# Kernel optimization log

Measured on AMD Instinct MI355X. Metric: run time of the kernel, lower is better.

## Reference

```python
import jax, jax.numpy as jnp
import numpy as np

N = 50000      # nodes
E = 1600000    # edges
M = 2          # modalities
DIN, H1, LAT, DEC, HID, NC = 2000, 500, 128, 64, 64, 16
EPS = 1e-5


def setup_inputs() -> dict:
    key = jax.random.key(0)
    ks = jax.random.split(key, 24)
    s = 0.02
    return {
        "x": jax.random.normal(ks[0], (M, N, DIN), jnp.float32),
        "src": jax.random.randint(ks[1], (E,), 0, N, jnp.int32),
        "dst": jax.random.randint(ks[2], (E,), 0, N, jnp.int32),
        "W1": jax.random.normal(ks[3], (M, DIN, H1), jnp.float32) * s,
        "b1": jax.random.normal(ks[4], (M, H1), jnp.float32) * s,
        "g1": jax.random.uniform(ks[5], (M, H1), jnp.float32) + 0.5,
        "be1": jax.random.normal(ks[6], (M, H1), jnp.float32) * s,
        "m1": jax.random.normal(ks[7], (M, H1), jnp.float32) * s,
        "v1": jax.random.uniform(ks[8], (M, H1), jnp.float32) + 0.5,
        "W2": jax.random.normal(ks[9], (M, H1, LAT), jnp.float32) * s,
        "b2": jax.random.normal(ks[10], (M, LAT), jnp.float32) * s,
        "g2": jax.random.uniform(ks[11], (M, LAT), jnp.float32) + 0.5,
        "be2": jax.random.normal(ks[12], (M, LAT), jnp.float32) * s,
        "m2": jax.random.normal(ks[13], (M, LAT), jnp.float32) * s,
        "v2": jax.random.uniform(ks[14], (M, LAT), jnp.float32) + 0.5,
        "Wd": jax.random.normal(ks[15], (M, LAT, DEC), jnp.float32) * s,
        "bd": jax.random.normal(ks[16], (M, DEC), jnp.float32) * s,
        "Wg1": jax.random.normal(ks[17], (DEC, HID), jnp.float32) * s,
        "bg1": jax.random.normal(ks[18], (HID,), jnp.float32) * s,
        "Wg2": jax.random.normal(ks[19], (HID, NC), jnp.float32) * s,
        "bg2": jax.random.normal(ks[20], (NC,), jnp.float32) * s,
    }


def _bn(h, g, b, m, v):
    # inference-mode BatchNorm1d; params broadcast over [M, 1, F]
    return (h - m[:, None, :]) * jax.lax.rsqrt(v[:, None, :] + EPS) * g[:, None, :] + b[:, None, :]


def reference(x, src, dst, W1, b1, g1, be1, m1, v1, W2, b2, g2, be2, m2, v2,
              Wd, bd, Wg1, bg1, Wg2, bg2):
    # --- multi-modal encoders (dropout = identity at eval) ---
    h = jnp.einsum('mnd,mdh->mnh', x, W1) + b1[:, None, :]        # [M,N,500]
    h = _bn(h, g1, be1, m1, v1)
    h = jnp.einsum('mnh,mhl->mnl', h, W2) + b2[:, None, :]        # [M,N,LAT]
    h = _bn(h, g2, be2, m2, v2)
    dec = jnp.einsum('mnl,mld->mnd', h, Wd) + bd[:, None, :]      # [M,N,DEC]
    node_features = jnp.mean(dec, axis=0)                         # [N,DEC]

    # --- GraphConv (DGL norm='both'): D_out^{-1/2} on src, D_in^{-1/2} on dst ---
    ones = jnp.ones(src.shape[0], jnp.float32)
    deg_out = jax.ops.segment_sum(ones, src, num_segments=N)
    deg_in = jax.ops.segment_sum(ones, dst, num_segments=N)
    c_src = jax.lax.rsqrt(jnp.clip(deg_out, 1.0))[:, None]
    c_dst = jax.lax.rsqrt(jnp.clip(deg_in, 1.0))[:, None]

    def gconv(feat, W, b):
        msg = (feat * c_src)[src]                                 # [E,F]
        agg = jax.ops.segment_sum(msg, dst, num_segments=N)       # [N,F]
        return (agg * c_dst) @ W + b

    h = jax.nn.relu(gconv(node_features, Wg1, bg1))               # [N,HID]
    score = gconv(h, Wg2, bg2)                                    # [N,NC]
    return score
```

## Files before the change

### kernel.cpp

```cpp
#include <hip/hip_runtime.h>

#define NN 50000
#define EE 1600000
#define MM 2
#define DIN 2000
#define H1 500
#define LAT 128
#define DECF 64
#define KTOT (MM*DIN)
#define KSTEPS (KTOT/32)
#define NTILES (NN/16)
#define GEMM_BLKS 768
#define DEG_BLKS 256
#define EPSBN 1e-5f

typedef float f32x4 __attribute__((ext_vector_type(4)));
typedef short short8v __attribute__((ext_vector_type(8)));
typedef unsigned int u32x2 __attribute__((ext_vector_type(2)));

__device__ __forceinline__ unsigned int pkbf(float a, float b){
  unsigned int ua = __float_as_uint(a), ub = __float_as_uint(b);
  ua = (ua + 0x7FFFu + ((ua>>16)&1u)) >> 16;
  ub = (ub + 0x7FFFu + ((ub>>16)&1u)) & 0xFFFF0000u;
  return ua | ub;
}
__device__ __forceinline__ unsigned short pk1(float a){
  unsigned int u = __float_as_uint(a);
  return (unsigned short)((u + 0x7FFFu + ((u>>16)&1u)) >> 16);
}
__device__ __forceinline__ float bfe0(unsigned int w){ return __uint_as_float(w<<16); }
__device__ __forceinline__ float bfe1(unsigned int w){ return __uint_as_float(w & 0xFFFF0000u); }

__global__ __launch_bounds__(256) void prepA(const float* __restrict__ W2,const float* __restrict__ Wd,
                      const float* __restrict__ g2,const float* __restrict__ v2,
                      float* __restrict__ T){
  __shared__ float a2[LAT];
  int m = (blockIdx.x*4) / H1;
  if (threadIdx.x < LAT)
    a2[threadIdx.x] = g2[m*LAT+threadIdx.x]*rsqrtf(v2[m*LAT+threadIdx.x]+EPSBN);
  __syncthreads();
  int g = blockIdx.x*256 + threadIdx.x;
  int d = g & 63; int mk = g >> 6; int k = mk % H1;
  const float* w2 = W2 + (size_t)(m*H1 + k)*LAT;
  const float* wd = Wd + (size_t)m*LAT*DECF + d;
  float acc = 0.f;
  for (int l = 0; l < LAT; ++l) acc += w2[l]*a2[l]*wd[(size_t)l*DECF];
  T[g] = acc;
}

__global__ __launch_bounds__(256) void prepB(const float* __restrict__ W1,const float* __restrict__ g1,
                      const float* __restrict__ v1,const float* __restrict__ T,
                      unsigned short* __restrict__ WB){
  __shared__ float a1[H1];
  int m = (blockIdx.x*4) / DIN;
  for (int k = threadIdx.x; k < H1; k += 256)
    a1[k] = g1[m*H1+k]*rsqrtf(v1[m*H1+k]+EPSBN);
  __syncthreads();
  int g = blockIdx.x*256 + threadIdx.x;
  int d = g & 63; int mi = g >> 6; int i = mi % DIN;
  const float* w1 = W1 + (size_t)(m*DIN + i)*H1;
  const float* t  = T + (size_t)m*H1*DECF + d;
  float acc = 0.f;
  for (int k = 0; k < H1; ++k) acc += w1[k]*a1[k]*t[(size_t)k*DECF];
  acc *= 0.5f;
  unsigned int u = __float_as_uint(acc);
  unsigned short bf = (unsigned short)((u + 0x7FFFu + ((u>>16)&1u)) >> 16);
  int kc = m*DIN + i;
  int s = kc >> 5, kl = kc & 31;
  int laneB = ((kl>>3)<<4) | (d & 15);
  int t4 = d >> 4;
  WB[((size_t)((s*4 + t4)*64 + laneB))*8 + (kl & 7)] = bf;
}

__global__ void prepC(const float* __restrict__ b1,const float* __restrict__ g1,const float* __restrict__ be1,
                      const float* __restrict__ m1,const float* __restrict__ v1,
                      const float* __restrict__ b2,const float* __restrict__ g2,const float* __restrict__ be2,
                      const float* __restrict__ m2,const float* __restrict__ v2,
                      const float* __restrict__ T,const float* __restrict__ Wd,
                      const float* __restrict__ bd, float* __restrict__ cbar){
  __shared__ float part[128];
  int d = threadIdx.x & 63, h = threadIdx.x >> 6;
  float s = 0.f;
  for (int m = 0; m < MM; ++m){
    if (h == 0) s += bd[m*DECF + d];
    const float* t = T + (size_t)m*H1*DECF + d;
    for (int k = h*(H1/2); k < (h+1)*(H1/2); ++k){
      float a = g1[m*H1+k]*rsqrtf(v1[m*H1+k]+EPSBN);
      float c = (b1[m*H1+k]-m1[m*H1+k])*a + be1[m*H1+k];
      s += c*t[(size_t)k*DECF];
    }
    const float* wd = Wd + (size_t)m*LAT*DECF + d;
    for (int l = h*(LAT/2); l < (h+1)*(LAT/2); ++l){
      float a = g2[m*LAT+l]*rsqrtf(v2[m*LAT+l]+EPSBN);
      float c = (b2[m*LAT+l]-m2[m*LAT+l])*a + be2[m*LAT+l];
      s += c*wd[(size_t)l*DECF];
    }
  }
  part[threadIdx.x] = s;
  __syncthreads();
  if (h == 0) cbar[d] = 0.5f*(part[d] + part[64+d]);
}

__global__ __launch_bounds__(1024) void scan1(const int* __restrict__ deg, int* __restrict__ rp,
                      int* __restrict__ bsum, int n){
  __shared__ int sm[1024];
  int i = blockIdx.x*1024 + threadIdx.x;
  int v = (i < n) ? deg[i] : 0;
  sm[threadIdx.x] = v; __syncthreads();
  for (int off=1; off<1024; off<<=1){
    int t = (threadIdx.x >= off) ? sm[threadIdx.x-off] : 0;
    __syncthreads();
    sm[threadIdx.x] += t;
    __syncthreads();
  }
  if (i < n) rp[i] = sm[threadIdx.x] - v;
  if (threadIdx.x == 1023) bsum[blockIdx.x] = sm[1023];
}

__global__ void scan3n(int* __restrict__ rp, const int* __restrict__ bsum,
                       const int* __restrict__ dout, const int* __restrict__ din,
                       float* __restrict__ csrc, float* __restrict__ cdst){
  int i = blockIdx.x*blockDim.x + threadIdx.x;
  if (i >= NN) return;
  int b = i >> 10;
  int base = 0;
  for (int j = 0; j < b; ++j) base += bsum[j];
  rp[i] += base;
  if (i == NN-1) rp[NN] = EE;
  int a = dout[i]; if (a < 1) a = 1;
  int dd = din[i]; if (dd < 1) dd = 1;
  csrc[i] = rsqrtf((float)a);
  cdst[i] = rsqrtf((float)dd);
}

__global__ void scatk(const int* __restrict__ src,const int* __restrict__ dst,
                      const int* __restrict__ rp,int* __restrict__ cur,int* __restrict__ ss){
  int e = blockIdx.x*blockDim.x + threadIdx.x;
  if (e >= EE) return;
  int d = dst[e];
  int p = rp[d] + atomicAdd(&cur[d], 1);
  ss[p] = src[e];
}

__global__ __launch_bounds__(256,4) void gemm_deg(
    const float* __restrict__ x, const short8v* __restrict__ WB,
    const float* __restrict__ cbar,
    unsigned short* __restrict__ nfb, int* __restrict__ ticket,
    const int* __restrict__ src, const int* __restrict__ dst,
    int* __restrict__ dout, int* __restrict__ din)
{
  if (blockIdx.x >= GEMM_BLKS){
    int t0 = (blockIdx.x - GEMM_BLKS)*256 + threadIdx.x;
    for (int e = t0; e < EE; e += 256*DEG_BLKS){
      atomicAdd(&dout[src[e]], 1);
      atomicAdd(&din[dst[e]], 1);
    }
    return;
  }
  const int lane = threadIdx.x & 63;
  const int r = lane & 15;
  const int kg = (lane >> 4) << 3;
  const int rg = (lane >> 4) << 2;
  const float cb0 = cbar[r], cb1 = cbar[16+r], cb2 = cbar[32+r], cb3 = cbar[48+r];

  while (true){
    int t = 0;
    if (lane == 0) t = atomicAdd(ticket, 1);
    t = __shfl(t, 0, 64);
    if (t >= NTILES) break;
    const int n0 = t*16;
    const float* xrow = x + (size_t)(n0 + r) * DIN;

    f32x4 acc0 = {0.f,0.f,0.f,0.f}, acc1 = acc0, acc2 = acc0, acc3 = acc0;
    f32x4 A0c, A1c; short8v B0c, B1c, B2c, B3c;
    {
      const float* p = xrow + kg;
      A0c = *(const f32x4*)p; A1c = *(const f32x4*)(p+4);
      const short8v* bp = WB + lane;
      B0c = bp[0]; B1c = bp[64]; B2c = bp[128]; B3c = bp[192];
    }
    for (int s = 0; s < KSTEPS-1; ++s){
      f32x4 A0n, A1n; short8v B0n, B1n, B2n, B3n;
      {
        int kr = (s+1)*32 + kg;
        const float* p = (kr < DIN) ? (xrow + kr)
                                    : (xrow + (size_t)(NN-1)*DIN + kr);
        A0n = *(const f32x4*)p; A1n = *(const f32x4*)(p+4);
        const short8v* bp = WB + (size_t)(s+1)*256 + lane;
        B0n = bp[0]; B1n = bp[64]; B2n = bp[128]; B3n = bp[192];
      }
      union { short8v v; unsigned int u[4]; } AF;
      AF.u[0]=pkbf(A0c[0],A0c[1]); AF.u[1]=pkbf(A0c[2],A0c[3]);
      AF.u[2]=pkbf(A1c[0],A1c[1]); AF.u[3]=pkbf(A1c[2],A1c[3]);
      acc0 = __builtin_amdgcn_mfma_f32_16x16x32_bf16(AF.v, B0c, acc0, 0,0,0);
      acc1 = __builtin_amdgcn_mfma_f32_16x16x32_bf16(AF.v, B1c, acc1, 0,0,0);
      acc2 = __builtin_amdgcn_mfma_f32_16x16x32_bf16(AF.v, B2c, acc2, 0,0,0);
      acc3 = __builtin_amdgcn_mfma_f32_16x16x32_bf16(AF.v, B3c, acc3, 0,0,0);
      A0c=A0n; A1c=A1n; B0c=B0n; B1c=B1n; B2c=B2n; B3c=B3n;
    }
    {
      union { short8v v; unsigned int u[4]; } AF;
      AF.u[0]=pkbf(A0c[0],A0c[1]); AF.u[1]=pkbf(A0c[2],A0c[3]);
      AF.u[2]=pkbf(A1c[0],A1c[1]); AF.u[3]=pkbf(A1c[2],A1c[3]);
      acc0 = __builtin_amdgcn_mfma_f32_16x16x32_bf16(AF.v, B0c, acc0, 0,0,0);
      acc1 = __builtin_amdgcn_mfma_f32_16x16x32_bf16(AF.v, B1c, acc1, 0,0,0);
      acc2 = __builtin_amdgcn_mfma_f32_16x16x32_bf16(AF.v, B2c, acc2, 0,0,0);
      acc3 = __builtin_amdgcn_mfma_f32_16x16x32_bf16(AF.v, B3c, acc3, 0,0,0);
    }
    #pragma unroll
    for (int rr = 0; rr < 4; ++rr){
      int rowD = n0 + rg + rr;
      unsigned short* o = nfb + (size_t)rowD*64 + r;
      o[0]  = pk1(acc0[rr] + cb0);
      o[16] = pk1(acc1[rr] + cb1);
      o[32] = pk1(acc2[rr] + cb2);
      o[48] = pk1(acc3[rr] + cb3);
    }
  }
}

__global__ __launch_bounds__(512,4) void fgd1(const unsigned short* __restrict__ nfb,
                      const int* __restrict__ rp,const int* __restrict__ ss,
                      const float* __restrict__ Wg1,const float* __restrict__ bg1,
                      const float* __restrict__ csrc,const float* __restrict__ cdst,
                      unsigned short* __restrict__ hpb){
  __shared__ float W[64*64];
  for (int i = threadIdx.x; i < 64*64; i += 512) W[i] = Wg1[i];
  __syncthreads();
  int wave = threadIdx.x >> 6, lane = threadIdx.x & 63;
  int q = lane >> 4, cc = (lane & 15)*4;
  const int NW = 512*8;
  for (int n = blockIdx.x*8 + wave; n < NN; n += NW){
    int beg = rp[n], end = rp[n+1];
    f32x4 s4 = {0.f,0.f,0.f,0.f};
    int e = beg + q;
    for (; e + 12 < end; e += 16){
      int i0 = ss[e], i1 = ss[e+4], i2 = ss[e+8], i3 = ss[e+12];
      float c0 = csrc[i0], c1 = csrc[i1], c2 = csrc[i2], c3 = csrc[i3];
      u32x2 w0 = *(const u32x2*)(nfb + (size_t)i0*64 + cc);
      u32x2 w1 = *(const u32x2*)(nfb + (size_t)i1*64 + cc);
      u32x2 w2 = *(const u32x2*)(nfb + (size_t)i2*64 + cc);
      u32x2 w3 = *(const u32x2*)(nfb + (size_t)i3*64 + cc);
      s4.x += c0*bfe0(w0.x) + c1*bfe0(w1.x) + c2*bfe0(w2.x) + c3*bfe0(w3.x);
      s4.y += c0*bfe1(w0.x) + c1*bfe1(w1.x) + c2*bfe1(w2.x) + c3*bfe1(w3.x);
      s4.z += c0*bfe0(w0.y) + c1*bfe0(w1.y) + c2*bfe0(w2.y) + c3*bfe0(w3.y);
      s4.w += c0*bfe1(w0.y) + c1*bfe1(w1.y) + c2*bfe1(w2.y) + c3*bfe1(w3.y);
    }
    for (; e < end; e += 4){
      int i0 = ss[e]; float c0 = csrc[i0];
      u32x2 w0 = *(const u32x2*)(nfb + (size_t)i0*64 + cc);
      s4.x += c0*bfe0(w0.x); s4.y += c0*bfe1(w0.x);
      s4.z += c0*bfe0(w0.y); s4.w += c0*bfe1(w0.y);
    }
    s4.x += __shfl_xor(s4.x,16); s4.y += __shfl_xor(s4.y,16);
    s4.z += __shfl_xor(s4.z,16); s4.w += __shfl_xor(s4.w,16);
    s4.x += __shfl_xor(s4.x,32); s4.y += __shfl_xor(s4.y,32);
    s4.z += __shfl_xor(s4.z,32); s4.w += __shfl_xor(s4.w,32);
    float acc = 0.f;
    #pragma unroll
    for (int l16 = 0; l16 < 16; ++l16){
      acc += __shfl(s4.x,l16) * W[(4*l16+0)*64 + lane];
      acc += __shfl(s4.y,l16) * W[(4*l16+1)*64 + lane];
      acc += __shfl(s4.z,l16) * W[(4*l16+2)*64 + lane];
      acc += __shfl(s4.w,l16) * W[(4*l16+3)*64 + lane];
    }
    float h = fmaxf(cdst[n]*acc + bg1[lane], 0.f) * csrc[n];
    hpb[(size_t)n*64 + lane] = pk1(h);
  }
}

__global__ __launch_bounds__(512,4) void fgd2(const unsigned short* __restrict__ hpb,
                      const int* __restrict__ rp,const int* __restrict__ ss,
                      const float* __restrict__ Wg2,const float* __restrict__ bg2,
                      const float* __restrict__ cdst,float* __restrict__ score){
  __shared__ float W[64*16];
  for (int i = threadIdx.x; i < 64*16; i += 512) W[i] = Wg2[i];
  __syncthreads();
  int wave = threadIdx.x >> 6, lane = threadIdx.x & 63;
  int q = lane >> 4, cc = (lane & 15)*4;
  const int NW = 512*8;
  for (int n = blockIdx.x*8 + wave; n < NN; n += NW){
    int beg = rp[n], end = rp[n+1];
    f32x4 s4 = {0.f,0.f,0.f,0.f};
    int e = beg + q;
    for (; e + 12 < end; e += 16){
      int i0 = ss[e], i1 = ss[e+4], i2 = ss[e+8], i3 = ss[e+12];
      u32x2 w0 = *(const u32x2*)(hpb + (size_t)i0*64 + cc);
      u32x2 w1 = *(const u32x2*)(hpb + (size_t)i1*64 + cc);
      u32x2 w2 = *(const u32x2*)(hpb + (size_t)i2*64 + cc);
      u32x2 w3 = *(const u32x2*)(hpb + (size_t)i3*64 + cc);
      s4.x += bfe0(w0.x) + bfe0(w1.x) + bfe0(w2.x) + bfe0(w3.x);
      s4.y += bfe1(w0.x) + bfe1(w1.x) + bfe1(w2.x) + bfe1(w3.x);
      s4.z += bfe0(w0.y) + bfe0(w1.y) + bfe0(w2.y) + bfe0(w3.y);
      s4.w += bfe1(w0.y) + bfe1(w1.y) + bfe1(w2.y) + bfe1(w3.y);
    }
    for (; e < end; e += 4){
      u32x2 w0 = *(const u32x2*)(hpb + (size_t)ss[e]*64 + cc);
      s4.x += bfe0(w0.x); s4.y += bfe1(w0.x);
      s4.z += bfe0(w0.y); s4.w += bfe1(w0.y);
    }
    s4.x += __shfl_xor(s4.x,16); s4.y += __shfl_xor(s4.y,16);
    s4.z += __shfl_xor(s4.z,16); s4.w += __shfl_xor(s4.w,16);
    s4.x += __shfl_xor(s4.x,32); s4.y += __shfl_xor(s4.y,32);
    s4.z += __shfl_xor(s4.z,32); s4.w += __shfl_xor(s4.w,32);
    int c = lane & 15;
    float acc = 0.f;
    #pragma unroll
    for (int l16 = 0; l16 < 16; ++l16){
      acc += __shfl(s4.x,l16) * W[(4*l16+0)*16 + c];
      acc += __shfl(s4.y,l16) * W[(4*l16+1)*16 + c];
      acc += __shfl(s4.z,l16) * W[(4*l16+2)*16 + c];
      acc += __shfl(s4.w,l16) * W[(4*l16+3)*16 + c];
    }
    if (lane < 16) score[(size_t)n*16 + lane] = cdst[n]*acc + bg2[lane];
  }
}

extern "C" void kernel_launch(void* const* d_in, const int* in_sizes, int n_in,
                              void* d_out, int out_size, void* d_ws, size_t ws_size,
                              hipStream_t stream){
  const float* x   = (const float*)d_in[0];
  const int* src   = (const int*)d_in[1];
  const int* dst   = (const int*)d_in[2];
  const float* W1  = (const float*)d_in[3];
  const float* b1  = (const float*)d_in[4];
  const float* g1  = (const float*)d_in[5];
  const float* be1 = (const float*)d_in[6];
  const float* m1  = (const float*)d_in[7];
  const float* v1  = (const float*)d_in[8];
  const float* W2  = (const float*)d_in[9];
  const float* b2  = (const float*)d_in[10];
  const float* g2  = (const float*)d_in[11];
  const float* be2 = (const float*)d_in[12];
  const float* m2  = (const float*)d_in[13];
  const float* v2  = (const float*)d_in[14];
  const float* Wd  = (const float*)d_in[15];
  const float* bd  = (const float*)d_in[16];
  const float* Wg1 = (const float*)d_in[17];
  const float* bg1 = (const float*)d_in[18];
  const float* Wg2 = (const float*)d_in[19];
  const float* bg2 = (const float*)d_in[20];
  float* score = (float*)d_out;

  char* w = (char*)d_ws;
  size_t off = 0;
  auto alc = [&](size_t b){ size_t c = off; off += (b + 255) & ~(size_t)255; return c; };
  size_t o_dout = alc((size_t)NN*4), o_din = alc((size_t)NN*4), o_cur = alc((size_t)NN*4);
  size_t o_tick = alc(256);
  size_t zspan = off;
  size_t o_rp  = alc((size_t)(NN+1)*4), o_bsum = alc(256*4);
  size_t o_csrc = alc((size_t)NN*4), o_cdst = alc((size_t)NN*4);
  size_t o_T = alc((size_t)MM*H1*DECF*4), o_cbar = alc(DECF*4);
  size_t o_WB = alc((size_t)MM*DIN*DECF*2);
  size_t o_ss = alc((size_t)EE*4);
  size_t o_nf = alc((size_t)NN*64*2);
  size_t o_hp = alc((size_t)NN*64*2);

  int* dout = (int*)(w+o_dout); int* din = (int*)(w+o_din); int* cur = (int*)(w+o_cur);
  int* tick = (int*)(w+o_tick);
  int* rp = (int*)(w+o_rp); int* bsum = (int*)(w+o_bsum);
  float* csrc = (float*)(w+o_csrc); float* cdst = (float*)(w+o_cdst);
  float* T = (float*)(w+o_T); float* cbar = (float*)(w+o_cbar);
  unsigned short* WBu = (unsigned short*)(w+o_WB);
  int* ss = (int*)(w+o_ss);
  unsigned short* nfb = (unsigned short*)(w+o_nf);
  unsigned short* hpb = (unsigned short*)(w+o_hp);

  hipMemsetAsync(w, 0, zspan, stream);

  prepA<<<(MM*H1*DECF)/256,256,0,stream>>>(W2,Wd,g2,v2,T);
  prepB<<<(MM*DIN*DECF)/256,256,0,stream>>>(W1,g1,v1,T,WBu);
  prepC<<<1,128,0,stream>>>(b1,g1,be1,m1,v1,b2,g2,be2,m2,v2,T,Wd,bd,cbar);

  gemm_deg<<<GEMM_BLKS+DEG_BLKS,256,0,stream>>>(x,(const short8v*)(w+o_WB),cbar,
                                                nfb,tick,src,dst,dout,din);

  int nb = (NN+1023)/1024;
  scan1<<<nb,1024,0,stream>>>(din,rp,bsum,NN);
  scan3n<<<(NN+255)/256,256,0,stream>>>(rp,bsum,dout,din,csrc,cdst);
  scatk<<<(EE+255)/256,256,0,stream>>>(src,dst,rp,cur,ss);

  fgd1<<<512,512,0,stream>>>(nfb,rp,ss,Wg1,bg1,csrc,cdst,hpb);
  fgd2<<<512,512,0,stream>>>(hpb,rp,ss,Wg2,bg2,cdst,score);
}
```

Before: 702.7 us.

## Statically assign GEMM tiles and fold degree counting into every block; dual-node gather

The fused GEMM kernel drops the atomic ticket work queue and separate degree-counting blocks. Each of 782 blocks now counts degrees for its own contiguous edge slice and then computes one 16-row tile per wave, statically assigned. The two graph-conv gather kernels now process two nodes per wave at once, interleaving their neighbor loads to expose more memory-level parallelism. The trade-offs are possible load imbalance without dynamic scheduling and higher register pressure in the gather kernels.

New measurement: 948.0 us. 1.35x slower.

```diff
diff --git a/kernel.cpp b/kernel.cpp
--- a/kernel.cpp
+++ b/kernel.cpp
@@ -10,8 +10,8 @@
 #define KTOT (MM*DIN)
 #define KSTEPS (KTOT/32)
 #define NTILES (NN/16)
-#define GEMM_BLKS 768
-#define DEG_BLKS 256
+#define GEMM_BLKS 782
+#define ESLICE ((EE + GEMM_BLKS - 1)/GEMM_BLKS)
 #define EPSBN 1e-5f
 
 typedef float f32x4 __attribute__((ext_vector_type(4)));
@@ -145,79 +145,90 @@
 __global__ __launch_bounds__(256,4) void gemm_deg(
     const float* __restrict__ x, const short8v* __restrict__ WB,
     const float* __restrict__ cbar,
-    unsigned short* __restrict__ nfb, int* __restrict__ ticket,
+    unsigned short* __restrict__ nfb,
     const int* __restrict__ src, const int* __restrict__ dst,
     int* __restrict__ dout, int* __restrict__ din)
 {
-  if (blockIdx.x >= GEMM_BLKS){
-    int t0 = (blockIdx.x - GEMM_BLKS)*256 + threadIdx.x;
-    for (int e = t0; e < EE; e += 256*DEG_BLKS){
+  {
+    int eBeg = blockIdx.x*ESLICE;
+    int eEnd = eBeg + ESLICE; if (eEnd > EE) eEnd = EE;
+    for (int e = eBeg + threadIdx.x; e < eEnd; e += 256){
       atomicAdd(&dout[src[e]], 1);
       atomicAdd(&din[dst[e]], 1);
     }
-    return;
-  }
+  }
+  const int t = blockIdx.x*4 + (threadIdx.x >> 6);
+  if (t >= NTILES) return;
   const int lane = threadIdx.x & 63;
   const int r = lane & 15;
   const int kg = (lane >> 4) << 3;
   const int rg = (lane >> 4) << 2;
   const float cb0 = cbar[r], cb1 = cbar[16+r], cb2 = cbar[32+r], cb3 = cbar[48+r];
-
-  while (true){
-    int t = 0;
-    if (lane == 0) t = atomicAdd(ticket, 1);
-    t = __shfl(t, 0, 64);
-    if (t >= NTILES) break;
-    const int n0 = t*16;
-    const float* xrow = x + (size_t)(n0 + r) * DIN;
-
-    f32x4 acc0 = {0.f,0.f,0.f,0.f}, acc1 = acc0, acc2 = acc0, acc3 = acc0;
-    f32x4 A0c, A1c; short8v B0c, B1c, B2c, B3c;
+  const int n0 = t*16;
+  const float* xrow = x + (size_t)(n0 + r) * DIN;
+
+  f32x4 acc0 = {0.f,0.f,0.f,0.f}, acc1 = acc0, acc2 = acc0, acc3 = acc0;
+  f32x4 A0c, A1c; short8v B0c, B1c, B2c, B3c;
+  {
+    const float* p = xrow + kg;
+    A0c = *(const f32x4*)p; A1c = *(const f32x4*)(p+4);
+    const short8v* bp = WB + lane;
+    B0c = bp[0]; B1c = bp[64]; B2c = bp[128]; B3c = bp[192];
+  }
+  for (int s = 0; s < KSTEPS-1; ++s){
+    f32x4 A0n, A1n; short8v B0n, B1n, B2n, B3n;
     {
-      const float* p = xrow + kg;
-      A0c = *(const f32x4*)p; A1c = *(const f32x4*)(p+4);
-      const short8v* bp = WB + lane;
-      B0c = bp[0]; B1c = bp[64]; B2c = bp[128]; B3c = bp[192];
-    }
-    for (int s = 0; s < KSTEPS-1; ++s){
-      f32x4 A0n, A1n; short8v B0n, B1n, B2n, B3n;
-      {
-        int kr = (s+1)*32 + kg;
-        const float* p = (kr < DIN) ? (xrow + kr)
-                                    : (xrow + (size_t)(NN-1)*DIN + kr);
-        A0n = *(const f32x4*)p; A1n = *(const f32x4*)(p+4);
-        const short8v* bp = WB + (size_t)(s+1)*256 + lane;
-        B0n = bp[0]; B1n = bp[64]; B2n = bp[128]; B3n = bp[192];
-      }
-      union { short8v v; unsigned int u[4]; } AF;
-      AF.u[0]=pkbf(A0c[0],A0c[1]); AF.u[1]=pkbf(A0c[2],A0c[3]);
-      AF.u[2]=pkbf(A1c[0],A1c[1]); AF.u[3]=pkbf(A1c[2],A1c[3]);
-      acc0 = __builtin_amdgcn_mfma_f32_16x16x32_bf16(AF.v, B0c, acc0, 0,0,0);
-      acc1 = __builtin_amdgcn_mfma_f32_16x16x32_bf16(AF.v, B1c, acc1, 0,0,0);
-      acc2 = __builtin_amdgcn_mfma_f32_16x16x32_bf16(AF.v, B2c, acc2, 0,0,0);
-      acc3 = __builtin_amdgcn_mfma_f32_16x16x32_bf16(AF.v, B3c, acc3, 0,0,0);
-      A0c=A0n; A1c=A1n; B0c=B0n; B1c=B1n; B2c=B2n; B3c=B3n;
-    }
-    {
-      union { short8v v; unsigned int u[4]; } AF;
-      AF.u[0]=pkbf(A0c[0],A0c[1]); AF.u[1]=pkbf(A0c[2],A0c[3]);
-      AF.u[2]=pkbf(A1c[0],A1c[1]); AF.u[3]=pkbf(A1c[2],A1c[3]);
-      acc0 = __builtin_amdgcn_mfma_f32_16x16x32_bf16(AF.v, B0c, acc0, 0,0,0);
-      acc1 = __builtin_amdgcn_mfma_f32_16x16x32_bf16(AF.v, B1c, acc1, 0,0,0);
-      acc2 = __builtin_amdgcn_mfma_f32_16x16x32_bf16(AF.v, B2c, acc2, 0,0,0);
-      acc3 = __builtin_amdgcn_mfma_f32_16x16x32_bf16(AF.v, B3c, acc3, 0,0,0);
-    }
-    #pragma unroll
-    for (int rr = 0; rr < 4; ++rr){
-      int rowD = n0 + rg + rr;
-      unsigned short* o = nfb + (size_t)rowD*64 + r;
-      o[0]  = pk1(acc0[rr] + cb0);
-      o[16] = pk1(acc1[rr] + cb1);
-      o[32] = pk1(acc2[rr] + cb2);
-      o[48] = pk1(acc3[rr] + cb3);
-    }
-  }
-}
+      int kr = (s+1)*32 + kg;
+      const float* p = (kr < DIN) ? (xrow + kr)
+                                  : (xrow + (size_t)(NN-1)*DIN + kr);
+      A0n = *(const f32x4*)p; A1n = *(const f32x4*)(p+4);
+      const short8v* bp = WB + (size_t)(s+1)*256 + lane;
+      B0n = bp[0]; B1n = bp[64]; B2n = bp[128]; B3n = bp[192];
+    }
+    union { short8v v; unsigned int u[4]; } AF;
+    AF.u[0]=pkbf(A0c[0],A0c[1]); AF.u[1]=pkbf(A0c[2],A0c[3]);
+    AF.u[2]=pkbf(A1c[0],A1c[1]); AF.u[3]=pkbf(A1c[2],A1c[3]);
+    acc0 = __builtin_amdgcn_mfma_f32_16x16x32_bf16(AF.v, B0c, acc0, 0,0,0);
+    acc1 = __builtin_amdgcn_mfma_f32_16x16x32_bf16(AF.v, B1c, acc1, 0,0,0);
+    acc2 = __builtin_amdgcn_mfma_f32_16x16x32_bf16(AF.v, B2c, acc2, 0,0,0);
+    acc3 = __builtin_amdgcn_mfma_f32_16x16x32_bf16(AF.v, B3c, acc3, 0,0,0);
+    A0c=A0n; A1c=A1n; B0c=B0n; B1c=B1n; B2c=B2n; B3c=B3n;
+  }
+  {
+    union { short8v v; unsigned int u[4]; } AF;
+    AF.u[0]=pkbf(A0c[0],A0c[1]); AF.u[1]=pkbf(A0c[2],A0c[3]);
+    AF.u[2]=pkbf(A1c[0],A1c[1]); AF.u[3]=pkbf(A1c[2],A1c[3]);
+    acc0 = __builtin_amdgcn_mfma_f32_16x16x32_bf16(AF.v, B0c, acc0, 0,0,0);
+    acc1 = __builtin_amdgcn_mfma_f32_16x16x32_bf16(AF.v, B1c, acc1, 0,0,0);
+    acc2 = __builtin_amdgcn_mfma_f32_16x16x32_bf16(AF.v, B2c, acc2, 0,0,0);
+    acc3 = __builtin_amdgcn_mfma_f32_16x16x32_bf16(AF.v, B3c, acc3, 0,0,0);
+  }
+  #pragma unroll
+  for (int rr = 0; rr < 4; ++rr){
+    int rowD = n0 + rg + rr;
+    unsigned short* o = nfb + (size_t)rowD*64 + r;
+    o[0]  = pk1(acc0[rr] + cb0);
+    o[16] = pk1(acc1[rr] + cb1);
+    o[32] = pk1(acc2[rr] + cb2);
+    o[48] = pk1(acc3[rr] + cb3);
+  }
+}
+
+#define ACC_CS(sv, idx) { float c_ = csrc[idx]; \
+  u32x2 w_ = *(const u32x2*)(nfb + (size_t)(idx)*64 + cc); \
+  sv.x += c_*bfe0(w_.x); sv.y += c_*bfe1(w_.x); \
+  sv.z += c_*bfe0(w_.y); sv.w += c_*bfe1(w_.y); }
+
+#define ACC_NC(sv, idx) { \
+  u32x2 w_ = *(const u32x2*)(hpb + (size_t)(idx)*64 + cc); \
+  sv.x += bfe0(w_.x); sv.y += bfe1(w_.x); \
+  sv.z += bfe0(w_.y); sv.w += bfe1(w_.y); }
+
+#define RED16(sv) \
+  sv.x += __shfl_xor(sv.x,16); sv.y += __shfl_xor(sv.y,16); \
+  sv.z += __shfl_xor(sv.z,16); sv.w += __shfl_xor(sv.w,16); \
+  sv.x += __shfl_xor(sv.x,32); sv.y += __shfl_xor(sv.y,32); \
+  sv.z += __shfl_xor(sv.z,32); sv.w += __shfl_xor(sv.w,32);
 
 __global__ __launch_bounds__(512,4) void fgd1(const unsigned short* __restrict__ nfb,
                       const int* __restrict__ rp,const int* __restrict__ ss,
@@ -229,43 +240,49 @@
   __syncthreads();
   int wave = threadIdx.x >> 6, lane = threadIdx.x & 63;
   int q = lane >> 4, cc = (lane & 15)*4;
-  const int NW = 512*8;
-  for (int n = blockIdx.x*8 + wave; n < NN; n += NW){
-    int beg = rp[n], end = rp[n+1];
-    f32x4 s4 = {0.f,0.f,0.f,0.f};
-    int e = beg + q;
-    for (; e + 12 < end; e += 16){
-      int i0 = ss[e], i1 = ss[e+4], i2 = ss[e+8], i3 = ss[e+12];
-      float c0 = csrc[i0], c1 = csrc[i1], c2 = csrc[i2], c3 = csrc[i3];
-      u32x2 w0 = *(const u32x2*)(nfb + (size_t)i0*64 + cc);
-      u32x2 w1 = *(const u32x2*)(nfb + (size_t)i1*64 + cc);
-      u32x2 w2 = *(const u32x2*)(nfb + (size_t)i2*64 + cc);
-      u32x2 w3 = *(const u32x2*)(nfb + (size_t)i3*64 + cc);
-      s4.x += c0*bfe0(w0.x) + c1*bfe0(w1.x) + c2*bfe0(w2.x) + c3*bfe0(w3.x);
-      s4.y += c0*bfe1(w0.x) + c1*bfe1(w1.x) + c2*bfe1(w2.x) + c3*bfe1(w3.x);
-      s4.z += c0*bfe0(w0.y) + c1*bfe0(w1.y) + c2*bfe0(w2.y) + c3*bfe0(w3.y);
-      s4.w += c0*bfe1(w0.y) + c1*bfe1(w1.y) + c2*bfe1(w2.y) + c3*bfe1(w3.y);
-    }
-    for (; e < end; e += 4){
-      int i0 = ss[e]; float c0 = csrc[i0];
-      u32x2 w0 = *(const u32x2*)(nfb + (size_t)i0*64 + cc);
-      s4.x += c0*bfe0(w0.x); s4.y += c0*bfe1(w0.x);
-      s4.z += c0*bfe0(w0.y); s4.w += c0*bfe1(w0.y);
-    }
-    s4.x += __shfl_xor(s4.x,16); s4.y += __shfl_xor(s4.y,16);
-    s4.z += __shfl_xor(s4.z,16); s4.w += __shfl_xor(s4.w,16);
-    s4.x += __shfl_xor(s4.x,32); s4.y += __shfl_xor(s4.y,32);
-    s4.z += __shfl_xor(s4.z,32); s4.w += __shfl_xor(s4.w,32);
-    float acc = 0.f;
+  const int WVS = 512*8;
+  int wid = blockIdx.x*8 + wave;
+  for (int n = wid; n < NN; n += 2*WVS){
+    int n2 = n + WVS;
+    bool has2 = (n2 < NN);
+    f32x4 sA = {0.f,0.f,0.f,0.f}, sB = sA;
+    int eA = rp[n] + q, endA = rp[n+1];
+    int eB = 0, endB = 0;
+    if (has2){ eB = rp[n2] + q; endB = rp[n2+1]; }
+    while (eA + 12 < endA && eB + 12 < endB){
+      int a0=ss[eA],a1=ss[eA+4],a2=ss[eA+8],a3=ss[eA+12];
+      int b0=ss[eB],b1=ss[eB+4],b2=ss[eB+8],b3=ss[eB+12];
+      ACC_CS(sA,a0); ACC_CS(sA,a1); ACC_CS(sA,a2); ACC_CS(sA,a3);
+      ACC_CS(sB,b0); ACC_CS(sB,b1); ACC_CS(sB,b2); ACC_CS(sB,b3);
+      eA += 16; eB += 16;
+    }
+    for (; eA + 12 < endA; eA += 16){
+      int a0=ss[eA],a1=ss[eA+4],a2=ss[eA+8],a3=ss[eA+12];
+      ACC_CS(sA,a0); ACC_CS(sA,a1); ACC_CS(sA,a2); ACC_CS(sA,a3);
+    }
+    for (; eB + 12 < endB; eB += 16){
+      int b0=ss[eB],b1=ss[eB+4],b2=ss[eB+8],b3=ss[eB+12];
+      ACC_CS(sB,b0); ACC_CS(sB,b1); ACC_CS(sB,b2); ACC_CS(sB,b3);
+    }
+    for (; eA < endA; eA += 4){ int a0 = ss[eA]; ACC_CS(sA,a0); }
+    for (; eB < endB; eB += 4){ int b0 = ss[eB]; ACC_CS(sB,b0); }
+    RED16(sA); RED16(sB);
+    float acc = 0.f, acc2 = 0.f;
     #pragma unroll
     for (int l16 = 0; l16 < 16; ++l16){
-      acc += __shfl(s4.x,l16) * W[(4*l16+0)*64 + lane];
-      acc += __shfl(s4.y,l16) * W[(4*l16+1)*64 + lane];
-      acc += __shfl(s4.z,l16) * W[(4*l16+2)*64 + lane];
-      acc += __shfl(s4.w,l16) * W[(4*l16+3)*64 + lane];
-    }
-    float h = fmaxf(cdst[n]*acc + bg1[lane], 0.f) * csrc[n];
-    hpb[(size_t)n*64 + lane] = pk1(h);
+      acc += __shfl(sA.x,l16) * W[(4*l16+0)*64 + lane];
+      acc += __shfl(sA.y,l16) * W[(4*l16+1)*64 + lane];
+      acc += __shfl(sA.z,l16) * W[(4*l16+2)*64 + lane];
+      acc += __shfl(sA.w,l16) * W[(4*l16+3)*64 + lane];
+      acc2 += __shfl(sB.x,l16) * W[(4*l16+0)*64 + lane];
+      acc2 += __shfl(sB.y,l16) * W[(4*l16+1)*64 + lane];
+      acc2 += __shfl(sB.z,l16) * W[(4*l16+2)*64 + lane];
+      acc2 += __shfl(sB.w,l16) * W[(4*l16+3)*64 + lane];
+    }
+    float bg = bg1[lane];
+    hpb[(size_t)n*64 + lane] = pk1(fmaxf(cdst[n]*acc + bg, 0.f) * csrc[n]);
+    if (has2)
+      hpb[(size_t)n2*64 + lane] = pk1(fmaxf(cdst[n2]*acc2 + bg, 0.f) * csrc[n2]);
   }
 }
 
@@ -278,41 +295,50 @@
   __syncthreads();
   int wave = threadIdx.x >> 6, lane = threadIdx.x & 63;
   int q = lane >> 4, cc = (lane & 15)*4;
-  const int NW = 512*8;
-  for (int n = blockIdx.x*8 + wave; n < NN; n += NW){
-    int beg = rp[n], end = rp[n+1];
-    f32x4 s4 = {0.f,0.f,0.f,0.f};
-    int e = beg + q;
-    for (; e + 12 < end; e += 16){
-      int i0 = ss[e], i1 = ss[e+4], i2 = ss[e+8], i3 = ss[e+12];
-      u32x2 w0 = *(const u32x2*)(hpb + (size_t)i0*64 + cc);
-      u32x2 w1 = *(const u32x2*)(hpb + (size_t)i1*64 + cc);
-      u32x2 w2 = *(const u32x2*)(hpb + (size_t)i2*64 + cc);
-      u32x2 w3 = *(const u32x2*)(hpb + (size_t)i3*64 + cc);
-      s4.x += bfe0(w0.x) + bfe0(w1.x) + bfe0(w2.x) + bfe0(w3.x);
-      s4.y += bfe1(w0.x) + bfe1(w1.x) + bfe1(w2.x) + bfe1(w3.x);
-      s4.z += bfe0(w0.y) + bfe0(w1.y) + bfe0(w2.y) + bfe0(w3.y);
-      s4.w += bfe1(w0.y) + bfe1(w1.y) + bfe1(w2.y) + bfe1(w3.y);
-    }
-    for (; e < end; e += 4){
-      u32x2 w0 = *(const u32x2*)(hpb + (size_t)ss[e]*64 + cc);
-      s4.x += bfe0(w0.x); s4.y += bfe1(w0.x);
-      s4.z += bfe0(w0.y); s4.w += bfe1(w0.y);
-    }
-    s4.x += __shfl_xor(s4.x,16); s4.y += __shfl_xor(s4.y,16);
-    s4.z += __shfl_xor(s4.z,16); s4.w += __shfl_xor(s4.w,16);
-    s4.x += __shfl_xor(s4.x,32); s4.y += __shfl_xor(s4.y,32);
-    s4.z += __shfl_xor(s4.z,32); s4.w += __shfl_xor(s4.w,32);
+  const int WVS = 512*8;
+  int wid = blockIdx.x*8 + wave;
+  for (int n = wid; n < NN; n += 2*WVS){
+    int n2 = n + WVS;
+    bool has2 = (n2 < NN);
+    f32x4 sA = {0.f,0.f,0.f,0.f}, sB = sA;
+    int eA = rp[n] + q, endA = rp[n+1];
+    int eB = 0, endB = 0;
+    if (has2){ eB = rp[n2] + q; endB = rp[n2+1]; }
+    while (eA + 12 < endA && eB + 12 < endB){
+      int a0=ss[eA],a1=ss[eA+4],a2=ss[eA+8],a3=ss[eA+12];
+      int b0=ss[eB],b1=ss[eB+4],b2=ss[eB+8],b3=ss[eB+12];
+      ACC_NC(sA,a0); ACC_NC(sA,a1); ACC_NC(sA,a2); ACC_NC(sA,a3);
+      ACC_NC(sB,b0); ACC_NC(sB,b1); ACC_NC(sB,b2); ACC_NC(sB,b3);
+      eA += 16; eB += 16;
+    }
+    for (; eA + 12 < endA; eA += 16){
+      int a0=ss[eA],a1=ss[eA+4],a2=ss[eA+8],a3=ss[eA+12];
+      ACC_NC(sA,a0); ACC_NC(sA,a1); ACC_NC(sA,a2); ACC_NC(sA,a3);
+    }
+    for (; eB + 12 < endB; eB += 16){
+      int b0=ss[eB],b1=ss[eB+4],b2=ss[eB+8],b3=ss[eB+12];
+      ACC_NC(sB,b0); ACC_NC(sB,b1); ACC_NC(sB,b2); ACC_NC(sB,b3);
+    }
+    for (; eA < endA; eA += 4){ int a0 = ss[eA]; ACC_NC(sA,a0); }
+    for (; eB < endB; eB += 4){ int b0 = ss[eB]; ACC_NC(sB,b0); }
+    RED16(sA); RED16(sB);
     int c = lane & 15;
-    float acc = 0.f;
+    float acc = 0.f, acc2 = 0.f;
     #pragma unroll
     for (int l16 = 0; l16 < 16; ++l16){
-      acc += __shfl(s4.x,l16) * W[(4*l16+0)*16 + c];
-      acc += __shfl(s4.y,l16) * W[(4*l16+1)*16 + c];
-      acc += __shfl(s4.z,l16) * W[(4*l16+2)*16 + c];
-      acc += __shfl(s4.w,l16) * W[(4*l16+3)*16 + c];
-    }
-    if (lane < 16) score[(size_t)n*16 + lane] = cdst[n]*acc + bg2[lane];
+      acc += __shfl(sA.x,l16) * W[(4*l16+0)*16 + c];
+      acc += __shfl(sA.y,l16) * W[(4*l16+1)*16 + c];
+      acc += __shfl(sA.z,l16) * W[(4*l16+2)*16 + c];
+      acc += __shfl(sA.w,l16) * W[(4*l16+3)*16 + c];
+      acc2 += __shfl(sB.x,l16) * W[(4*l16+0)*16 + c];
+      acc2 += __shfl(sB.y,l16) * W[(4*l16+1)*16 + c];
+      acc2 += __shfl(sB.z,l16) * W[(4*l16+2)*16 + c];
+      acc2 += __shfl(sB.w,l16) * W[(4*l16+3)*16 + c];
+    }
+    if (lane < 16){
+      score[(size_t)n*16 + lane] = cdst[n]*acc + bg2[lane];
+      if (has2) score[(size_t)n2*16 + lane] = cdst[n2]*acc2 + bg2[lane];
+    }
   }
 }
 
@@ -346,7 +372,6 @@
   size_t off = 0;
   auto alc = [&](size_t b){ size_t c = off; off += (b + 255) & ~(size_t)255; return c; };
   size_t o_dout = alc((size_t)NN*4), o_din = alc((size_t)NN*4), o_cur = alc((size_t)NN*4);
-  size_t o_tick = alc(256);
   size_t zspan = off;
   size_t o_rp  = alc((size_t)(NN+1)*4), o_bsum = alc(256*4);
   size_t o_csrc = alc((size_t)NN*4), o_cdst = alc((size_t)NN*4);
@@ -357,7 +382,6 @@
   size_t o_hp = alc((size_t)NN*64*2);
 
   int* dout = (int*)(w+o_dout); int* din = (int*)(w+o_din); int* cur = (int*)(w+o_cur);
-  int* tick = (int*)(w+o_tick);
   int* rp = (int*)(w+o_rp); int* bsum = (int*)(w+o_bsum);
   float* csrc = (float*)(w+o_csrc); float* cdst = (float*)(w+o_cdst);
   float* T = (float*)(w+o_T); float* cbar = (float*)(w+o_cbar);
@@ -365,15 +389,16 @@
   int* ss = (int*)(w+o_ss);
   unsigned short* nfb = (unsigned short*)(w+o_nf);
   unsigned short* hpb = (unsigned short*)(w+o_hp);
+  (void)WBu;
 
   hipMemsetAsync(w, 0, zspan, stream);
 
   prepA<<<(MM*H1*DECF)/256,256,0,stream>>>(W2,Wd,g2,v2,T);
-  prepB<<<(MM*DIN*DECF)/256,256,0,stream>>>(W1,g1,v1,T,WBu);
+  prepB<<<(MM*DIN*DECF)/256,256,0,stream>>>(W1,g1,v1,T,(unsigned short*)(w+o_WB));
   prepC<<<1,128,0,stream>>>(b1,g1,be1,m1,v1,b2,g2,be2,m2,v2,T,Wd,bd,cbar);
 
-  gemm_deg<<<GEMM_BLKS+DEG_BLKS,256,0,stream>>>(x,(const short8v*)(w+o_WB),cbar,
-                                                nfb,tick,src,dst,dout,din);
+  gemm_deg<<<GEMM_BLKS,256,0,stream>>>(x,(const short8v*)(w+o_WB),cbar,
+                                       nfb,src,dst,dout,din);
 
   int nb = (NN+1023)/1024;
   scan1<<<nb,1024,0,stream>>>(din,rp,bsum,NN);
```
